# Optimization experiments

Measured on AMD Instinct MI355X. Metric: run time of the kernel, lower is better.

Reference implementation:

```python
import jax, jax.numpy as jnp
import numpy as np

N_TOKENS = 3
EMBED = 10
RNN = 10
N_LABELS = 3
B = 16384
T = 99
EPS = 1e-7  # keras CategoricalCrossentropy clip epsilon


def setup_inputs() -> dict:
    key = jax.random.key(0)
    ks = jax.random.split(key, 8)
    token_ids = jax.random.randint(ks[0], (B, T), 0, N_TOKENS, dtype=jnp.int32)
    label_ids = jax.random.randint(ks[1], (B, T), 0, N_LABELS)
    labels = jax.nn.one_hot(label_ids, N_LABELS, dtype=jnp.float32)
    mask = jnp.ones((B, T), dtype=bool)  # accepted by call() but unused, kept for signature fidelity
    emb_table = jax.random.normal(ks[2], (N_TOKENS, EMBED), jnp.float32) * 0.05
    W = jax.random.normal(ks[3], (EMBED, RNN), jnp.float32) / np.sqrt(EMBED)
    U = jax.random.normal(ks[4], (RNN, RNN), jnp.float32) / np.sqrt(RNN)
    b = jnp.zeros((RNN,), jnp.float32)
    Wo = jax.random.normal(ks[5], (RNN, N_LABELS), jnp.float32) / np.sqrt(RNN)
    bo = jnp.zeros((N_LABELS,), jnp.float32)
    return dict(token_ids=token_ids, labels=labels, mask=mask,
                emb_table=emb_table, W=W, U=U, b=b, Wo=Wo, bo=bo)


def reference(token_ids, labels, mask, emb_table, W, U, b, Wo, bo):
    # Embedding lookup (mask_zero=True -> token 0 is a masked step)
    emb = emb_table[token_ids]                      # [B, T, E]
    step_mask = (token_ids != 0)                    # [B, T]

    def step(h, inp):
        x_t, m_t = inp                              # [B, E], [B]
        h_new = jnp.tanh(x_t @ W + h @ U + b)       # SimpleRNN cell
        # Keras masking: masked timesteps carry previous state/output
        h = jnp.where(m_t[:, None], h_new, h)
        return h, h

    h0 = jnp.zeros((token_ids.shape[0], W.shape[1]), emb.dtype)
    _, states_tb = jax.lax.scan(step, h0, (emb.transpose(1, 0, 2), step_mask.T))
    states = states_tb.transpose(1, 0, 2)           # [B, T, R]

    probs = jax.nn.softmax(states @ Wo + bo, axis=-1)   # Dense(softmax) -> [B, T, L]
    probs_c = jnp.clip(probs, EPS, 1.0)
    loss = jnp.mean(-jnp.sum(labels * jnp.log(probs_c), axis=-1))
    accuracy = jnp.mean((jnp.argmax(probs, axis=-1) == jnp.argmax(labels, axis=-1)).astype(jnp.float32))
    return states, probs, accuracy, loss
```

## Files before the change

### kernel.cpp

```cpp
#include <hip/hip_runtime.h>
#include <math.h>

#define BB 16384
#define TT 99
#define RR 10
#define LL 3

#define QP(v, j) __int_as_float(__builtin_amdgcn_mov_dpp(                     \
    __float_as_int(v), (j) * 0x55, 0xF, 0xF, true))
#define HMIR(v)  __int_as_float(__builtin_amdgcn_mov_dpp(                     \
    __float_as_int(v), 0x141, 0xF, 0xF, true))

__device__ __forceinline__ void gather10(float hoA, float hoB, float (&hg)[RR]) {
    hg[0] = QP(hoA, 0); hg[1] = QP(hoA, 1);
    hg[2] = QP(hoA, 2); hg[3] = QP(hoA, 3);
    const float mr = HMIR(hoA);
    hg[4] = QP(mr, 0);  hg[5] = QP(mr, 1);
    hg[6] = QP(mr, 2);  hg[7] = QP(mr, 3);
    hg[8] = QP(hoB, 0); hg[9] = QP(hoB, 1);
}

__device__ __forceinline__ void logit_step(
    const float (&hg)[RR], int yv, int tep, int g,
    const float (&Wc)[RR], float boc, float* __restrict__ srow)
{
    float lg = boc;
#pragma unroll
    for (int i = 0; i < RR; ++i) lg = fmaf(hg[i], Wc[i], lg);
    if (g == 0) lg = __int_as_float((__float_as_int(lg) & ~3) | yv);
    if (g < 3) srow[tep * LL + g] = lg;
}

template <int TB, int N>
__device__ __forceinline__ void rnn_section(
    uint64_t wsel, uint64_t wy, float& hoA, float& hoB,
    const float (&UA)[RR], const float (&UB)[RR],
    const float (&Wc)[RR], float boc,
    float cA1, float cA2, float cB1, float cB2,
    float* __restrict__ outA, float* __restrict__ outB,
    float* __restrict__ srow, int g)
{
#pragma unroll
    for (int u = 0; u < N; ++u) {
        const int sel = (int)(wsel & 3); wsel >>= 2;
        const int yv  = (int)(wy & 3);   wy >>= 2;

        float hg[RR];
        gather10(hoA, hoB, hg);

        if (TB + u > 0)
            logit_step(hg, yv, TB + u - 1, g, Wc, boc, srow);

        const bool is1 = (sel == 1);
        float aA0 = is1 ? cA1 : cA2, aB0 = is1 ? cB1 : cB2;
        float aA1 = 0.0f, aB1 = 0.0f;
#pragma unroll
        for (int i = 0; i < 5; ++i) {
            aA0 = fmaf(hg[i],     UA[i],     aA0);
            aA1 = fmaf(hg[5 + i], UA[5 + i], aA1);
            aB0 = fmaf(hg[i],     UB[i],     aB0);
            aB1 = fmaf(hg[5 + i], UB[5 + i], aB1);
        }
        const float eA = __expf(2.0f * (aA0 + aA1));
        const float eB = __expf(2.0f * (aB0 + aB1));
        const float pA = eA + 1.0f, pB = eB + 1.0f;
        const float r  = __builtin_amdgcn_rcpf(pA * pB);
        const float hnA = fmaf(-2.0f * pB, r, 1.0f);
        const float hnB = fmaf(-2.0f * pA, r, 1.0f);
        if (sel != 0) { hoA = hnA; hoB = hnB; }

        outA[(TB + u) * RR] = hoA;
        if (g < 2) outB[(TB + u) * RR] = hoB;
    }
}

__global__ __launch_bounds__(256, 2)
void rnn_seq_kernel(const int* __restrict__ tok_ids,
                    const float* __restrict__ labels,
                    const float* __restrict__ emb,
                    const float* __restrict__ W,
                    const float* __restrict__ U,
                    const float* __restrict__ bvec,
                    const float* __restrict__ Wo,
                    const float* __restrict__ bo,
                    float* __restrict__ states_out,
                    float* __restrict__ logits_out)
{
    __shared__ __align__(16) float   s_lg[4][8 * TT * LL];
    __shared__ unsigned char         s_code[4][8 * 100];

    const int tid = threadIdx.x;
    const int w   = tid >> 6;
    const int l   = tid & 63;
    const int r8  = l >> 3;
    const int g   = l & 7;
    const int rowbase = blockIdx.x * 32 + w * 8;

#pragma unroll
    for (int i = 0; i < 13; ++i) {
        const int p = l + 64 * i;
        if (p < 8 * TT) {
            const size_t gi = (size_t)rowbase * TT + p;
            const int   tk  = tok_ids[gi];
            const float la1 = labels[gi * LL + 1];
            const float la2 = labels[gi * LL + 2];
            const int   y   = (la1 > 0.5f) ? 1 : ((la2 > 0.5f) ? 2 : 0);
            const int   r   = p / TT;
            s_code[w][r * 100 + (p - r * TT)] = (unsigned char)((tk << 2) | y);
        }
    }

    const unsigned char* cp = &s_code[w][r8 * 100];
    uint64_t sw0 = 0, sw1 = 0, sw2 = 0, sw3 = 0;
    uint64_t yw0 = 0, yw1 = 0, yw2 = 0, yw3 = 0;
#pragma unroll
    for (int t = 0; t < TT; ++t) {
        const uint64_t c  = (uint64_t)cp[t];
        const uint64_t sv = (c >> 2) & 3, yv = c & 3;
        if (t < 32)              sw0 |= sv << (2 * t);
        else if (t < 64)         sw1 |= sv << (2 * (t - 32));
        else if (t < 96)         sw2 |= sv << (2 * (t - 64));
        else                     sw3 |= sv << (2 * (t - 96));
        const int s2 = t + 1;
        if (s2 < 32)             yw0 |= yv << (2 * s2);
        else if (s2 < 64)        yw1 |= yv << (2 * (s2 - 32));
        else if (s2 < 96)        yw2 |= yv << (2 * (s2 - 64));
        else                     yw3 |= yv << (2 * (s2 - 96));
    }
    const int y98 = (int)((yw3 >> 6) & 3);

    const int qpar = g >> 2;
    int ord[8];
#pragma unroll
    for (int j = 0; j < 4; ++j) {
        ord[j]     = qpar ? 4 + j : j;
        ord[4 + j] = qpar ? 3 - j : 7 - j;
    }
    const int jA = g;
    const int jB = ((g & 3) < 2) ? 8 + (g & 3) : 8;
    const int gc = ((g & 3) < 2) ? (g & 3) : 2;

    float UA[RR], UB[RR], Wc[RR];
#pragma unroll
    for (int k2 = 0; k2 < 8; ++k2) {
        UA[k2] = U[ord[k2] * RR + jA];
        UB[k2] = U[ord[k2] * RR + jB];
        Wc[k2] = Wo[ord[k2] * LL + gc];
    }
    UA[8] = U[8 * RR + jA]; UA[9] = U[9 * RR + jA];
    UB[8] = U[8 * RR + jB]; UB[9] = U[9 * RR + jB];
    Wc[8] = Wo[8 * LL + gc]; Wc[9] = Wo[9 * LL + gc];
    const float boc = bo[gc];

    float cA1 = bvec[jA], cA2 = cA1, cB1 = bvec[jB], cB2 = cB1;
#pragma unroll
    for (int i = 0; i < RR; ++i) {
        const float e1 = emb[RR + i];
        const float e2 = emb[2 * RR + i];
        const float wA = W[i * RR + jA];
        const float wB = W[i * RR + jB];
        cA1 = fmaf(e1, wA, cA1); cA2 = fmaf(e2, wA, cA2);
        cB1 = fmaf(e1, wB, cB1); cB2 = fmaf(e2, wB, cB2);
    }

    const int row = rowbase + r8;
    float* outA = states_out + (size_t)row * (TT * RR) + jA;
    float* outB = states_out + (size_t)row * (TT * RR) + jB;
    float* srow = &s_lg[w][r8 * (TT * LL)];

    float hoA = 0.0f, hoB = 0.0f;

    rnn_section< 0, 32>(sw0, yw0, hoA, hoB, UA, UB, Wc, boc,
                        cA1, cA2, cB1, cB2, outA, outB, srow, g);
    rnn_section<32, 32>(sw1, yw1, hoA, hoB, UA, UB, Wc, boc,
                        cA1, cA2, cB1, cB2, outA, outB, srow, g);
    rnn_section<64, 32>(sw2, yw2, hoA, hoB, UA, UB, Wc, boc,
                        cA1, cA2, cB1, cB2, outA, outB, srow, g);
    rnn_section<96,  3>(sw3, yw3, hoA, hoB, UA, UB, Wc, boc,
                        cA1, cA2, cB1, cB2, outA, outB, srow, g);

    {
        float hg[RR];
        gather10(hoA, hoB, hg);
        logit_step(hg, y98, 98, g, Wc, boc, srow);
    }

    {
        const float4* s4 = reinterpret_cast<const float4*>(&s_lg[w][0]);
        float4* d4 = reinterpret_cast<float4*>(
            logits_out + (size_t)rowbase * (TT * LL));
#pragma unroll
        for (int i = 0; i < 10; ++i) {
            const int q = l + 64 * i;
            if (q < 594) d4[q] = s4[q];
        }
    }
}

__global__ __launch_bounds__(256)
void softmax_kernel(float* __restrict__ probs,
                    float* __restrict__ ws)
{
    const int NT     = BB * TT;
    const int tid    = blockIdx.x * 256 + threadIdx.x;
    const int stride = 2048 * 256;

    float loss = 0.0f;
    int   corr = 0;

#pragma unroll 1
    for (int idx = tid; idx < NT; idx += stride) {
        float* pp = probs + (size_t)idx * LL;
        const float l0 = pp[0], l1 = pp[1], l2 = pp[2];
        const int   y  = __float_as_int(l0) & 3;

        const float e0 = __expf(l0), e1 = __expf(l1), e2 = __expf(l2);
        const float S  = e0 + e1 + e2;
        const float rs = __builtin_amdgcn_rcpf(S);
        pp[0] = e0 * rs; pp[1] = e1 * rs; pp[2] = e2 * rs;

        const float ly = (y == 0) ? l0 : ((y == 1) ? l1 : l2);
        loss += fminf(__logf(S) - ly, 16.11809565f);

        int ap = 0; float pm = l0;
        if (l1 > pm) { ap = 1; pm = l1; }
        if (l2 > pm) { ap = 2; }
        corr += (ap == y) ? 1 : 0;
    }

    __shared__ float sl[4], sc[4];
    float ls = loss, cs = (float)corr;
#pragma unroll
    for (int off = 32; off > 0; off >>= 1) {
        ls += __shfl_down(ls, off, 64);
        cs += __shfl_down(cs, off, 64);
    }
    if ((threadIdx.x & 63) == 0) { sl[threadIdx.x >> 6] = ls; sc[threadIdx.x >> 6] = cs; }
    __syncthreads();
    if (threadIdx.x == 0) {
        ws[blockIdx.x]        = sl[0] + sl[1] + sl[2] + sl[3];
        ws[2048 + blockIdx.x] = sc[0] + sc[1] + sc[2] + sc[3];
    }
}

__global__ __launch_bounds__(256)
void finalize_kernel(const float* __restrict__ ws, float* __restrict__ out_tail)
{
    __shared__ float sl[4], sc[4];
    const int t = threadIdx.x;
    float ls = 0.0f, cs = 0.0f;
#pragma unroll
    for (int i = 0; i < 8; ++i) {
        ls += ws[t + 256 * i];
        cs += ws[2048 + t + 256 * i];
    }
#pragma unroll
    for (int off = 32; off > 0; off >>= 1) {
        ls += __shfl_down(ls, off, 64);
        cs += __shfl_down(cs, off, 64);
    }
    if ((t & 63) == 0) { sl[t >> 6] = ls; sc[t >> 6] = cs; }
    __syncthreads();
    if (t == 0) {
        const float L = sl[0] + sl[1] + sl[2] + sl[3];
        const float C = sc[0] + sc[1] + sc[2] + sc[3];
        const float inv = 1.0f / (float)((size_t)BB * TT);
        out_tail[0] = C * inv;
        out_tail[1] = L * inv;
    }
}

extern "C" void kernel_launch(void* const* d_in, const int* in_sizes, int n_in,
                              void* d_out, int out_size, void* d_ws, size_t ws_size,
                              hipStream_t stream)
{
    const int*   tok    = (const int*)  d_in[0];
    const float* labels = (const float*)d_in[1];
    const float* emb = (const float*)d_in[3];
    const float* W   = (const float*)d_in[4];
    const float* U   = (const float*)d_in[5];
    const float* bv  = (const float*)d_in[6];
    const float* Wo  = (const float*)d_in[7];
    const float* bo  = (const float*)d_in[8];

    float* out    = (float*)d_out;
    float* states = out;
    float* probs  = out + (size_t)BB * TT * RR;
    float* tail   = out + (size_t)BB * TT * (RR + LL);
    float* ws     = (float*)d_ws;

    rnn_seq_kernel<<<BB / 32, 256, 0, stream>>>(tok, labels, emb, W, U, bv,
                                                Wo, bo, states, probs);
    softmax_kernel<<<2048, 256, 0, stream>>>(probs, ws);
    finalize_kernel<<<1, 256, 0, stream>>>(ws, tail);
}
```

Measured before the change: 52.29 us.

## Split RNN recurrence into checkpoint pass and segment-parallel replay pass

The single sequential RNN kernel is replaced by two kernels. The first runs the recurrence for the first 66 steps and stores only the hidden-state checkpoints at steps 32 and 65. The second launches three times as many blocks, one per 33-step segment, each restarting from its checkpoint to write states and logits. This exposes more parallelism than the 512 blocks of the original, at the cost of recomputing two thirds of the recurrence, an extra launch, and a dependency through global memory.

Result: slower. 64.53 us (+23.4%).

```diff
diff --git a/kernel.cpp b/kernel.cpp
--- a/kernel.cpp
+++ b/kernel.cpp
@@ -5,6 +5,7 @@
 #define TT 99
 #define RR 10
 #define LL 3
+#define SEG 33
 
 #define QP(v, j) __int_as_float(__builtin_amdgcn_mov_dpp(                     \
     __float_as_int(v), (j) * 0x55, 0xF, 0xF, true))
@@ -20,115 +21,46 @@
     hg[8] = QP(hoB, 0); hg[9] = QP(hoB, 1);
 }
 
-__device__ __forceinline__ void logit_step(
-    const float (&hg)[RR], int yv, int tep, int g,
+__device__ __forceinline__ void rnn_update(
+    int sel, float& hoA, float& hoB, const float (&hg)[RR],
+    const float (&UA)[RR], const float (&UB)[RR],
+    float cA1, float cA2, float cB1, float cB2)
+{
+    const bool is1 = (sel == 1);
+    float aA0 = is1 ? cA1 : cA2, aB0 = is1 ? cB1 : cB2;
+    float aA1 = 0.0f, aB1 = 0.0f;
+#pragma unroll
+    for (int i = 0; i < 5; ++i) {
+        aA0 = fmaf(hg[i],     UA[i],     aA0);
+        aA1 = fmaf(hg[5 + i], UA[5 + i], aA1);
+        aB0 = fmaf(hg[i],     UB[i],     aB0);
+        aB1 = fmaf(hg[5 + i], UB[5 + i], aB1);
+    }
+    const float eA = __expf(2.0f * (aA0 + aA1));
+    const float eB = __expf(2.0f * (aB0 + aB1));
+    const float pA = eA + 1.0f, pB = eB + 1.0f;
+    const float r  = __builtin_amdgcn_rcpf(pA * pB);
+    const float hnA = fmaf(-2.0f * pB, r, 1.0f);
+    const float hnB = fmaf(-2.0f * pA, r, 1.0f);
+    if (sel != 0) { hoA = hnA; hoB = hnB; }
+}
+
+__device__ __forceinline__ void logit_emit(
+    const float (&hg)[RR], int yv, int u, int g,
     const float (&Wc)[RR], float boc, float* __restrict__ srow)
 {
     float lg = boc;
 #pragma unroll
     for (int i = 0; i < RR; ++i) lg = fmaf(hg[i], Wc[i], lg);
     if (g == 0) lg = __int_as_float((__float_as_int(lg) & ~3) | yv);
-    if (g < 3) srow[tep * LL + g] = lg;
-}
-
-template <int TB, int N>
-__device__ __forceinline__ void rnn_section(
-    uint64_t wsel, uint64_t wy, float& hoA, float& hoB,
-    const float (&UA)[RR], const float (&UB)[RR],
-    const float (&Wc)[RR], float boc,
-    float cA1, float cA2, float cB1, float cB2,
-    float* __restrict__ outA, float* __restrict__ outB,
-    float* __restrict__ srow, int g)
-{
-#pragma unroll
-    for (int u = 0; u < N; ++u) {
-        const int sel = (int)(wsel & 3); wsel >>= 2;
-        const int yv  = (int)(wy & 3);   wy >>= 2;
-
-        float hg[RR];
-        gather10(hoA, hoB, hg);
-
-        if (TB + u > 0)
-            logit_step(hg, yv, TB + u - 1, g, Wc, boc, srow);
-
-        const bool is1 = (sel == 1);
-        float aA0 = is1 ? cA1 : cA2, aB0 = is1 ? cB1 : cB2;
-        float aA1 = 0.0f, aB1 = 0.0f;
-#pragma unroll
-        for (int i = 0; i < 5; ++i) {
-            aA0 = fmaf(hg[i],     UA[i],     aA0);
-            aA1 = fmaf(hg[5 + i], UA[5 + i], aA1);
-            aB0 = fmaf(hg[i],     UB[i],     aB0);
-            aB1 = fmaf(hg[5 + i], UB[5 + i], aB1);
-        }
-        const float eA = __expf(2.0f * (aA0 + aA1));
-        const float eB = __expf(2.0f * (aB0 + aB1));
-        const float pA = eA + 1.0f, pB = eB + 1.0f;
-        const float r  = __builtin_amdgcn_rcpf(pA * pB);
-        const float hnA = fmaf(-2.0f * pB, r, 1.0f);
-        const float hnB = fmaf(-2.0f * pA, r, 1.0f);
-        if (sel != 0) { hoA = hnA; hoB = hnB; }
-
-        outA[(TB + u) * RR] = hoA;
-        if (g < 2) outB[(TB + u) * RR] = hoB;
-    }
-}
-
-__global__ __launch_bounds__(256, 2)
-void rnn_seq_kernel(const int* __restrict__ tok_ids,
-                    const float* __restrict__ labels,
-                    const float* __restrict__ emb,
-                    const float* __restrict__ W,
-                    const float* __restrict__ U,
-                    const float* __restrict__ bvec,
-                    const float* __restrict__ Wo,
-                    const float* __restrict__ bo,
-                    float* __restrict__ states_out,
-                    float* __restrict__ logits_out)
-{
-    __shared__ __align__(16) float   s_lg[4][8 * TT * LL];
-    __shared__ unsigned char         s_code[4][8 * 100];
-
-    const int tid = threadIdx.x;
-    const int w   = tid >> 6;
-    const int l   = tid & 63;
-    const int r8  = l >> 3;
-    const int g   = l & 7;
-    const int rowbase = blockIdx.x * 32 + w * 8;
-
-#pragma unroll
-    for (int i = 0; i < 13; ++i) {
-        const int p = l + 64 * i;
-        if (p < 8 * TT) {
-            const size_t gi = (size_t)rowbase * TT + p;
-            const int   tk  = tok_ids[gi];
-            const float la1 = labels[gi * LL + 1];
-            const float la2 = labels[gi * LL + 2];
-            const int   y   = (la1 > 0.5f) ? 1 : ((la2 > 0.5f) ? 2 : 0);
-            const int   r   = p / TT;
-            s_code[w][r * 100 + (p - r * TT)] = (unsigned char)((tk << 2) | y);
-        }
-    }
-
-    const unsigned char* cp = &s_code[w][r8 * 100];
-    uint64_t sw0 = 0, sw1 = 0, sw2 = 0, sw3 = 0;
-    uint64_t yw0 = 0, yw1 = 0, yw2 = 0, yw3 = 0;
-#pragma unroll
-    for (int t = 0; t < TT; ++t) {
-        const uint64_t c  = (uint64_t)cp[t];
-        const uint64_t sv = (c >> 2) & 3, yv = c & 3;
-        if (t < 32)              sw0 |= sv << (2 * t);
-        else if (t < 64)         sw1 |= sv << (2 * (t - 32));
-        else if (t < 96)         sw2 |= sv << (2 * (t - 64));
-        else                     sw3 |= sv << (2 * (t - 96));
-        const int s2 = t + 1;
-        if (s2 < 32)             yw0 |= yv << (2 * s2);
-        else if (s2 < 64)        yw1 |= yv << (2 * (s2 - 32));
-        else if (s2 < 96)        yw2 |= yv << (2 * (s2 - 64));
-        else                     yw3 |= yv << (2 * (s2 - 96));
-    }
-    const int y98 = (int)((yw3 >> 6) & 3);
-
+    if (g < 3) srow[u * LL + g] = lg;
+}
+
+__device__ __forceinline__ void setup_weights(
+    int g, const float* U, const float* W, const float* emb, const float* bvec,
+    float (&UA)[RR], float (&UB)[RR], int& jA, int& jB,
+    float& cA1, float& cA2, float& cB1, float& cB2)
+{
     const int qpar = g >> 2;
     int ord[8];
 #pragma unroll
@@ -136,23 +68,17 @@
         ord[j]     = qpar ? 4 + j : j;
         ord[4 + j] = qpar ? 3 - j : 7 - j;
     }
-    const int jA = g;
-    const int jB = ((g & 3) < 2) ? 8 + (g & 3) : 8;
-    const int gc = ((g & 3) < 2) ? (g & 3) : 2;
-
-    float UA[RR], UB[RR], Wc[RR];
+    jA = g;
+    jB = ((g & 3) < 2) ? 8 + (g & 3) : 8;
 #pragma unroll
     for (int k2 = 0; k2 < 8; ++k2) {
         UA[k2] = U[ord[k2] * RR + jA];
         UB[k2] = U[ord[k2] * RR + jB];
-        Wc[k2] = Wo[ord[k2] * LL + gc];
     }
     UA[8] = U[8 * RR + jA]; UA[9] = U[9 * RR + jA];
     UB[8] = U[8 * RR + jB]; UB[9] = U[9 * RR + jB];
-    Wc[8] = Wo[8 * LL + gc]; Wc[9] = Wo[9 * LL + gc];
-    const float boc = bo[gc];
-
-    float cA1 = bvec[jA], cA2 = cA1, cB1 = bvec[jB], cB2 = cB1;
+
+    cA1 = bvec[jA]; cA2 = cA1; cB1 = bvec[jB]; cB2 = cB1;
 #pragma unroll
     for (int i = 0; i < RR; ++i) {
         const float e1 = emb[RR + i];
@@ -162,37 +88,191 @@
         cA1 = fmaf(e1, wA, cA1); cA2 = fmaf(e2, wA, cA2);
         cB1 = fmaf(e1, wB, cB1); cB2 = fmaf(e2, wB, cB2);
     }
+}
+
+__global__ __launch_bounds__(256, 2)
+void rnn_pass1(const int* __restrict__ tok_ids,
+               const float* __restrict__ emb,
+               const float* __restrict__ W,
+               const float* __restrict__ U,
+               const float* __restrict__ bvec,
+               float* __restrict__ states_out)
+{
+    __shared__ unsigned char s_tk[4][8 * 66];
+
+    const int tid = threadIdx.x;
+    const int w   = tid >> 6;
+    const int l   = tid & 63;
+    const int r8  = l >> 3;
+    const int g   = l & 7;
+    const int rowbase = blockIdx.x * 32 + w * 8;
+
+#pragma unroll
+    for (int i = 0; i < 9; ++i) {
+        const int p = l + 64 * i;
+        if (p < 8 * 66) {
+            const int r = p / 66;
+            const int t = p - r * 66;
+            s_tk[w][r * 66 + t] =
+                (unsigned char)tok_ids[(size_t)(rowbase + r) * TT + t];
+        }
+    }
+
+    const unsigned char* cp = &s_tk[w][r8 * 66];
+    uint64_t w0 = 0, w1 = 0;
+#pragma unroll
+    for (int t = 0; t < 32; ++t)
+        w0 |= (uint64_t)(cp[t] & 3) << (2 * t);
+    const int s32 = (int)cp[32];
+#pragma unroll
+    for (int t = 33; t < 65; ++t)
+        w1 |= (uint64_t)(cp[t] & 3) << (2 * (t - 33));
+    const int s65 = (int)cp[65];
+
+    float UA[RR], UB[RR];
+    int jA, jB;
+    float cA1, cA2, cB1, cB2;
+    setup_weights(g, U, W, emb, bvec, UA, UB, jA, jB, cA1, cA2, cB1, cB2);
 
     const int row = rowbase + r8;
     float* outA = states_out + (size_t)row * (TT * RR) + jA;
     float* outB = states_out + (size_t)row * (TT * RR) + jB;
-    float* srow = &s_lg[w][r8 * (TT * LL)];
 
     float hoA = 0.0f, hoB = 0.0f;
 
-    rnn_section< 0, 32>(sw0, yw0, hoA, hoB, UA, UB, Wc, boc,
-                        cA1, cA2, cB1, cB2, outA, outB, srow, g);
-    rnn_section<32, 32>(sw1, yw1, hoA, hoB, UA, UB, Wc, boc,
-                        cA1, cA2, cB1, cB2, outA, outB, srow, g);
-    rnn_section<64, 32>(sw2, yw2, hoA, hoB, UA, UB, Wc, boc,
-                        cA1, cA2, cB1, cB2, outA, outB, srow, g);
-    rnn_section<96,  3>(sw3, yw3, hoA, hoB, UA, UB, Wc, boc,
-                        cA1, cA2, cB1, cB2, outA, outB, srow, g);
-
+#pragma unroll
+    for (int u = 0; u < 32; ++u) {
+        const int sel = (int)(w0 & 3); w0 >>= 2;
+        float hg[RR]; gather10(hoA, hoB, hg);
+        rnn_update(sel, hoA, hoB, hg, UA, UB, cA1, cA2, cB1, cB2);
+    }
+    { float hg[RR]; gather10(hoA, hoB, hg);
+      rnn_update(s32, hoA, hoB, hg, UA, UB, cA1, cA2, cB1, cB2); }
+    outA[32 * RR] = hoA;
+    if (g < 2) outB[32 * RR] = hoB;
+#pragma unroll
+    for (int u = 0; u < 32; ++u) {
+        const int sel = (int)(w1 & 3); w1 >>= 2;
+        float hg[RR]; gather10(hoA, hoB, hg);
+        rnn_update(sel, hoA, hoB, hg, UA, UB, cA1, cA2, cB1, cB2);
+    }
+    { float hg[RR]; gather10(hoA, hoB, hg);
+      rnn_update(s65, hoA, hoB, hg, UA, UB, cA1, cA2, cB1, cB2); }
+    outA[65 * RR] = hoA;
+    if (g < 2) outB[65 * RR] = hoB;
+}
+
+__global__ __launch_bounds__(256, 6)
+void rnn_pass2(const int* __restrict__ tok_ids,
+               const float* __restrict__ labels,
+               const float* __restrict__ emb,
+               const float* __restrict__ W,
+               const float* __restrict__ U,
+               const float* __restrict__ bvec,
+               const float* __restrict__ Wo,
+               const float* __restrict__ bo,
+               float* __restrict__ states_out,
+               float* __restrict__ logits_out)
+{
+    __shared__ __align__(8) float   s_lg[4][8 * SEG * LL];
+    __shared__ unsigned char        s_code[4][8 * 34];
+
+    const int seg  = blockIdx.x / 512;
+    const int rbk  = blockIdx.x - seg * 512;
+    const int base = seg * SEG;
+
+    const int tid = threadIdx.x;
+    const int w   = tid >> 6;
+    const int l   = tid & 63;
+    const int r8  = l >> 3;
+    const int g   = l & 7;
+    const int rowbase = rbk * 32 + w * 8;
+
+#pragma unroll
+    for (int i = 0; i < 5; ++i) {
+        const int p = l + 64 * i;
+        if (p < 8 * 33) {
+            const int r = p / 33;
+            const int t = p - r * 33;
+            const size_t gi = (size_t)(rowbase + r) * TT + base + t;
+            const int   tk  = tok_ids[gi];
+            const float la1 = labels[gi * LL + 1];
+            const float la2 = labels[gi * LL + 2];
+            const int   y   = (la1 > 0.5f) ? 1 : ((la2 > 0.5f) ? 2 : 0);
+            s_code[w][r * 34 + t] = (unsigned char)((tk << 2) | y);
+        }
+    }
+
+    const unsigned char* cp = &s_code[w][r8 * 34];
+    uint64_t wsel = 0, wy = 0;
+#pragma unroll
+    for (int u = 0; u < 32; ++u)
+        wsel |= (uint64_t)((cp[u] >> 2) & 3) << (2 * u);
+    const int s32 = (int)((cp[32] >> 2) & 3);
+#pragma unroll
+    for (int u = 1; u < 32; ++u)
+        wy |= (uint64_t)(cp[u - 1] & 3) << (2 * u);
+    const int y31 = (int)(cp[31] & 3);
+    const int y32 = (int)(cp[32] & 3);
+
+    float UA[RR], UB[RR];
+    int jA, jB;
+    float cA1, cA2, cB1, cB2;
+    setup_weights(g, U, W, emb, bvec, UA, UB, jA, jB, cA1, cA2, cB1, cB2);
+
+    const int qpar = g >> 2;
+    const int gc = ((g & 3) < 2) ? (g & 3) : 2;
+    float Wc[RR];
+#pragma unroll
+    for (int j = 0; j < 4; ++j) {
+        const int o0 = qpar ? 4 + j : j;
+        const int o1 = qpar ? 3 - j : 7 - j;
+        Wc[j]     = Wo[o0 * LL + gc];
+        Wc[4 + j] = Wo[o1 * LL + gc];
+    }
+    Wc[8] = Wo[8 * LL + gc]; Wc[9] = Wo[9 * LL + gc];
+    const float boc = bo[gc];
+
+    const int row = rowbase + r8;
+    float* outA = states_out + (size_t)row * (TT * RR) + base * RR + jA;
+    float* outB = states_out + (size_t)row * (TT * RR) + base * RR + jB;
+    float* srow = &s_lg[w][r8 * (SEG * LL)];
+
+    float hoA = 0.0f, hoB = 0.0f;
+    if (seg > 0) {
+        const size_t ck = (size_t)row * (TT * RR) + (size_t)(base - 1) * RR;
+        hoA = states_out[ck + jA];
+        hoB = states_out[ck + jB];
+    }
+
+#pragma unroll
+    for (int u = 0; u < 32; ++u) {
+        const int sel = (int)(wsel & 3); wsel >>= 2;
+        const int yv  = (int)(wy & 3);   wy >>= 2;
+        float hg[RR]; gather10(hoA, hoB, hg);
+        if (u > 0) logit_emit(hg, yv, u - 1, g, Wc, boc, srow);
+        rnn_update(sel, hoA, hoB, hg, UA, UB, cA1, cA2, cB1, cB2);
+        outA[u * RR] = hoA;
+        if (g < 2) outB[u * RR] = hoB;
+    }
     {
-        float hg[RR];
-        gather10(hoA, hoB, hg);
-        logit_step(hg, y98, 98, g, Wc, boc, srow);
-    }
-
-    {
-        const float4* s4 = reinterpret_cast<const float4*>(&s_lg[w][0]);
-        float4* d4 = reinterpret_cast<float4*>(
-            logits_out + (size_t)rowbase * (TT * LL));
-#pragma unroll
-        for (int i = 0; i < 10; ++i) {
-            const int q = l + 64 * i;
-            if (q < 594) d4[q] = s4[q];
+        float hg[RR]; gather10(hoA, hoB, hg);
+        logit_emit(hg, y31, 31, g, Wc, boc, srow);
+        rnn_update(s32, hoA, hoB, hg, UA, UB, cA1, cA2, cB1, cB2);
+        outA[32 * RR] = hoA;
+        if (g < 2) outB[32 * RR] = hoB;
+        float hg2[RR]; gather10(hoA, hoB, hg2);
+        logit_emit(hg2, y32, 32, g, Wc, boc, srow);
+    }
+
+#pragma unroll
+    for (int i = 0; i < 13; ++i) {
+        const int q = l + 64 * i;
+        if (q < 8 * SEG * LL) {
+            const int r = q / 99;
+            const int m = q - r * 99;
+            logits_out[(size_t)(rowbase + r) * (TT * LL) + base * LL + m] =
+                s_lg[w][r * 99 + m];
         }
     }
 }
@@ -289,8 +369,9 @@
     float* tail   = out + (size_t)BB * TT * (RR + LL);
     float* ws     = (float*)d_ws;
 
-    rnn_seq_kernel<<<BB / 32, 256, 0, stream>>>(tok, labels, emb, W, U, bv,
-                                                Wo, bo, states, probs);
+    rnn_pass1<<<512, 256, 0, stream>>>(tok, emb, W, U, bv, states);
+    rnn_pass2<<<1536, 256, 0, stream>>>(tok, labels, emb, W, U, bv, Wo, bo,
+                                        states, probs);
     softmax_kernel<<<2048, 256, 0, stream>>>(probs, ws);
     finalize_kernel<<<1, 256, 0, stream>>>(ws, tail);
 }
```
